# Performance work log

Hardware: AMD Instinct MI355X
Metric: run time of the kernel (lower is better)

Reference implementation:

```python
import jax, jax.numpy as jnp
import numpy as np

N_CELLTYPE = 50
M_PER_CT = 2000     # features per celltype
N_FEATURE = 20000
N_CELL = 512


def setup_inputs() -> dict:
    key = jax.random.key(0)
    k1, k2, k3 = jax.random.split(key, 3)
    x = jax.random.normal(k1, (N_FEATURE, N_CELL), dtype=jnp.float32)
    # nn.init.normal_(w, 1.0, 0.1)
    weight = 1.0 + 0.1 * jax.random.normal(k2, (N_CELLTYPE,), dtype=jnp.float32)
    idx = jax.random.randint(k3, (N_CELLTYPE, M_PER_CT), 0, N_FEATURE, dtype=jnp.int64)
    return {"x": x, "weight": weight, "idx": idx}


def reference(x, weight, idx):
    # Fused equivalent of: for each celltype ii, gather x[idx[ii]] * weight[ii],
    # vstack all, then flatten(transpose(.)).
    n_ct, m = idx.shape
    z = x[idx.reshape(-1)] * jnp.repeat(weight, m)[:, None]  # [n_ct*m, n_cell]
    return z.T.reshape(-1)  # flatten(t(z)), row-major over transposed matrix
```

## Files before the change

kernel.cpp:

```cpp
#include <hip/hip_runtime.h>

#define N_CELLTYPE 50
#define M_PER_CT   2000
#define N_FEATURE  20000
#define N_CELL     512
#define R_TOTAL    (N_CELLTYPE * M_PER_CT)
#define TR         32
#define TC         256
#define NTHREADS   512

typedef float vfloat4 __attribute__((ext_vector_type(4)));

__global__ __launch_bounds__(NTHREADS) void ct_scale_transpose(
    const float* __restrict__ x, const float* __restrict__ w,
    const int* __restrict__ idx, float* __restrict__ out) {
  __shared__ float tile[TR][TC + 4];
  __shared__ int   srow[TR];
  __shared__ float sw[TR];

  const int r0 = blockIdx.x * TR;
  const int c0 = blockIdx.y * TC;
  const int t  = threadIdx.x;

  if (t < TR) {
    const int r = r0 + t;
    srow[t] = idx[r];
    sw[t]   = w[r / M_PER_CT];
  }
  __syncthreads();

#pragma unroll
  for (int i = 0; i < 4; ++i) {
    const int linear = i * NTHREADS + t;
    const int row = linear >> 6;
    const int q   = linear & 63;
    const float4 v = *reinterpret_cast<const float4*>(
        x + (long)srow[row] * N_CELL + c0 + q * 4);
    const float s = sw[row];
    float4 sv;
    sv.x = v.x * s; sv.y = v.y * s; sv.z = v.z * s; sv.w = v.w * s;
    *reinterpret_cast<float4*>(&tile[row][q * 4]) = sv;
  }
  __syncthreads();

#pragma unroll
  for (int i = 0; i < 4; ++i) {
    const int linear = i * NTHREADS + t;
    const int c  = linear >> 3;
    const int q  = linear & 7;
    const int rr = q * 4;
    vfloat4 v;
    v.x = tile[rr + 0][c];
    v.y = tile[rr + 1][c];
    v.z = tile[rr + 2][c];
    v.w = tile[rr + 3][c];
    __builtin_nontemporal_store(
        v, reinterpret_cast<vfloat4*>(out + (long)(c0 + c) * R_TOTAL + r0 + rr));
  }
}

extern "C" void kernel_launch(void* const* d_in, const int* in_sizes, int n_in,
                              void* d_out, int out_size, void* d_ws, size_t ws_size,
                              hipStream_t stream) {
  const float* x   = (const float*)d_in[0];
  const float* w   = (const float*)d_in[1];
  const int*   idx = (const int*)d_in[2];
  float*       out = (float*)d_out;

  dim3 grid(R_TOTAL / TR, N_CELL / TC);
  ct_scale_transpose<<<grid, NTHREADS, 0, stream>>>(x, w, idx, out);
}
```

Baseline: 246.6 us.

## Reshape transpose tile to 256 rows by 32 columns with XOR-swizzled LDS

Changes the tile from 32 gathered rows by 256 columns to 256 rows by 32 columns, so each output row write becomes a 1 KB contiguous run instead of 128-byte chunks. It stores the tile column-major in LDS with an XOR swizzle so the transpose readback is a single float4 LDS load per thread, and adds bounds guards because 100000 is not a multiple of 256. In exchange, each gathered x row is read as only 128-byte segments, which may hurt read coalescing, and the LDS writes become scalar.

```diff
diff --git a/kernel.cpp b/kernel.cpp
--- a/kernel.cpp
+++ b/kernel.cpp
@@ -5,16 +5,17 @@
 #define N_FEATURE  20000
 #define N_CELL     512
 #define R_TOTAL    (N_CELLTYPE * M_PER_CT)
-#define TR         32
-#define TC         256
+#define TR         256
+#define TC         32
 #define NTHREADS   512
+#define NRT        ((R_TOTAL + TR - 1) / TR)
 
 typedef float vfloat4 __attribute__((ext_vector_type(4)));
 
 __global__ __launch_bounds__(NTHREADS) void ct_scale_transpose(
     const float* __restrict__ x, const float* __restrict__ w,
     const int* __restrict__ idx, float* __restrict__ out) {
-  __shared__ float tile[TR][TC + 4];
+  __shared__ float tile[TC][TR];
   __shared__ int   srow[TR];
   __shared__ float sw[TR];
 
@@ -24,38 +25,46 @@
 
   if (t < TR) {
     const int r = r0 + t;
-    srow[t] = idx[r];
-    sw[t]   = w[r / M_PER_CT];
+    if (r < R_TOTAL) {
+      srow[t] = idx[r];
+      sw[t]   = w[r / M_PER_CT];
+    } else {
+      srow[t] = 0;
+      sw[t]   = 0.0f;
+    }
   }
   __syncthreads();
 
 #pragma unroll
   for (int i = 0; i < 4; ++i) {
     const int linear = i * NTHREADS + t;
-    const int row = linear >> 6;
-    const int q   = linear & 63;
+    const int row = linear >> 3;
+    const int q   = linear & 7;
     const float4 v = *reinterpret_cast<const float4*>(
         x + (long)srow[row] * N_CELL + c0 + q * 4);
     const float s = sw[row];
-    float4 sv;
-    sv.x = v.x * s; sv.y = v.y * s; sv.z = v.z * s; sv.w = v.w * s;
-    *reinterpret_cast<float4*>(&tile[row][q * 4]) = sv;
+    const float e[4] = {v.x * s, v.y * s, v.z * s, v.w * s};
+#pragma unroll
+    for (int j = 0; j < 4; ++j) {
+      const int c    = q * 4 + j;
+      const int rswz = row ^ (((c >> 1) & 7) << 2);
+      tile[c][rswz] = e[j];
+    }
   }
   __syncthreads();
 
 #pragma unroll
   for (int i = 0; i < 4; ++i) {
     const int linear = i * NTHREADS + t;
-    const int c  = linear >> 3;
-    const int q  = linear & 7;
-    const int rr = q * 4;
-    vfloat4 v;
-    v.x = tile[rr + 0][c];
-    v.y = tile[rr + 1][c];
-    v.z = tile[rr + 2][c];
-    v.w = tile[rr + 3][c];
-    __builtin_nontemporal_store(
-        v, reinterpret_cast<vfloat4*>(out + (long)(c0 + c) * R_TOTAL + r0 + rr));
+    const int c    = linear >> 6;
+    const int lane = linear & 63;
+    const int m    = lane ^ ((c >> 1) & 7);
+    const int r    = r0 + lane * 4;
+    if (r < R_TOTAL) {
+      const vfloat4 v = *reinterpret_cast<const vfloat4*>(&tile[c][m * 4]);
+      __builtin_nontemporal_store(
+          v, reinterpret_cast<vfloat4*>(out + (long)(c0 + c) * R_TOTAL + r));
+    }
   }
 }
 
@@ -67,6 +76,6 @@
   const int*   idx = (const int*)d_in[2];
   float*       out = (float*)d_out;
 
-  dim3 grid(R_TOTAL / TR, N_CELL / TC);
+  dim3 grid(NRT, N_CELL / TC);
   ct_scale_transpose<<<grid, NTHREADS, 0, stream>>>(x, w, idx, out);
 }
```

Measured after the change: 243.1 us. About the same (-1.4%).

## Stage two x columns in LDS per block and gather rows from shared memory

Applied to the files above, without the earlier changes.

The kernel is rebuilt so that each of 256 blocks loads two full columns of x (all 20000 features) into about 160KB of LDS. It then walks the whole index array, gathering from LDS and writing two contiguous output rows with vector nontemporal stores. This replaces the repeated global gather of full x rows plus a shared-memory transpose tile with a single pass over x, and makes the output writes fully coalesced. The trade-offs are that only one block fits per CU, the column loads are narrow 8-byte strided reads, the load phase does not overlap with the store phase, and every block rereads the full idx array.

```diff
diff --git a/kernel.cpp b/kernel.cpp
--- a/kernel.cpp
+++ b/kernel.cpp
@@ -5,57 +5,52 @@
 #define N_FEATURE  20000
 #define N_CELL     512
 #define R_TOTAL    (N_CELLTYPE * M_PER_CT)
-#define TR         32
-#define TC         256
-#define NTHREADS   512
+#define NTHREADS   1024
+#define NBLOCKS    (N_CELL / 2)
 
 typedef float vfloat4 __attribute__((ext_vector_type(4)));
 
-__global__ __launch_bounds__(NTHREADS) void ct_scale_transpose(
+__global__ __launch_bounds__(NTHREADS) void ct_colpair(
     const float* __restrict__ x, const float* __restrict__ w,
     const int* __restrict__ idx, float* __restrict__ out) {
-  __shared__ float tile[TR][TC + 4];
-  __shared__ int   srow[TR];
-  __shared__ float sw[TR];
+  __shared__ float xl[N_FEATURE * 2];
+  __shared__ float sw[N_CELLTYPE];
 
-  const int r0 = blockIdx.x * TR;
-  const int c0 = blockIdx.y * TC;
+  const int b  = blockIdx.x;
+  const int c0 = 2 * ((b & 7) * 32 + (b >> 3));
   const int t  = threadIdx.x;
 
-  if (t < TR) {
-    const int r = r0 + t;
-    srow[t] = idx[r];
-    sw[t]   = w[r / M_PER_CT];
+  if (t < N_CELLTYPE) sw[t] = w[t];
+
+#pragma unroll
+  for (int i = 0; i < 20; ++i) {
+    const int f = i * NTHREADS + t;
+    if (f < N_FEATURE) {
+      const float2 v =
+          *reinterpret_cast<const float2*>(x + (long)f * N_CELL + c0);
+      *reinterpret_cast<float2*>(&xl[f * 2]) = v;
+    }
   }
   __syncthreads();
 
-#pragma unroll
-  for (int i = 0; i < 4; ++i) {
-    const int linear = i * NTHREADS + t;
-    const int row = linear >> 6;
-    const int q   = linear & 63;
-    const float4 v = *reinterpret_cast<const float4*>(
-        x + (long)srow[row] * N_CELL + c0 + q * 4);
-    const float s = sw[row];
-    float4 sv;
-    sv.x = v.x * s; sv.y = v.y * s; sv.z = v.z * s; sv.w = v.w * s;
-    *reinterpret_cast<float4*>(&tile[row][q * 4]) = sv;
-  }
-  __syncthreads();
-
-#pragma unroll
-  for (int i = 0; i < 4; ++i) {
-    const int linear = i * NTHREADS + t;
-    const int c  = linear >> 3;
-    const int q  = linear & 7;
-    const int rr = q * 4;
-    vfloat4 v;
-    v.x = tile[rr + 0][c];
-    v.y = tile[rr + 1][c];
-    v.z = tile[rr + 2][c];
-    v.w = tile[rr + 3][c];
-    __builtin_nontemporal_store(
-        v, reinterpret_cast<vfloat4*>(out + (long)(c0 + c) * R_TOTAL + r0 + rr));
+  float* o0 = out + (long)c0 * R_TOTAL;
+  float* o1 = o0 + R_TOTAL;
+#pragma unroll 2
+  for (int rb = 0; rb < R_TOTAL; rb += NTHREADS * 4) {
+    const int r = rb + t * 4;
+    if (r < R_TOTAL) {
+      const int4 f4 = *reinterpret_cast<const int4*>(idx + r);
+      const float s = sw[r / M_PER_CT];
+      const float2 g0 = *reinterpret_cast<const float2*>(&xl[f4.x * 2]);
+      const float2 g1 = *reinterpret_cast<const float2*>(&xl[f4.y * 2]);
+      const float2 g2 = *reinterpret_cast<const float2*>(&xl[f4.z * 2]);
+      const float2 g3 = *reinterpret_cast<const float2*>(&xl[f4.w * 2]);
+      vfloat4 v0, v1;
+      v0.x = g0.x * s; v0.y = g1.x * s; v0.z = g2.x * s; v0.w = g3.x * s;
+      v1.x = g0.y * s; v1.y = g1.y * s; v1.z = g2.y * s; v1.w = g3.y * s;
+      __builtin_nontemporal_store(v0, reinterpret_cast<vfloat4*>(o0 + r));
+      __builtin_nontemporal_store(v1, reinterpret_cast<vfloat4*>(o1 + r));
+    }
   }
 }
 
@@ -67,6 +62,5 @@
   const int*   idx = (const int*)d_in[2];
   float*       out = (float*)d_out;
 
-  dim3 grid(R_TOTAL / TR, N_CELL / TC);
-  ct_scale_transpose<<<grid, NTHREADS, 0, stream>>>(x, w, idx, out);
+  ct_colpair<<<dim3(NBLOCKS), dim3(NTHREADS), 0, stream>>>(x, w, idx, out);
 }
```

Result: slower. 259.2 us (+5.1%).
